# Kernel optimization log

Hardware: AMD Instinct MI355X
Metric: run time of the kernel (lower is better)

## Reference

```python
import jax, jax.numpy as jnp
import numpy as np

ROPE_THETA = 10000.0

def rope(x):
    # RoPE over the FULL model_dim (applied pre head-split, as in the source),
    # interleaved even/odd pairs. x: [B, S, D]
    B, S, D = x.shape
    half = D // 2
    inv_freq = 1.0 / (ROPE_THETA ** (jnp.arange(half, dtype=jnp.float32) * 2.0 / D))
    ang = jnp.arange(S, dtype=jnp.float32)[:, None] * inv_freq[None, :]  # [S, half]
    cos, sin = jnp.cos(ang), jnp.sin(ang)
    x1, x2 = x[..., 0::2], x[..., 1::2]
    r1 = x1 * cos - x2 * sin
    r2 = x1 * sin + x2 * cos
    return jnp.stack([r1, r2], axis=-1).reshape(B, S, D)


def setup_inputs() -> dict:
    key = jax.random.key(0)
    ks = jax.random.split(key, 9)
    B, S, D = 4, 2048, 768
    w = 0.02
    return {
        "X":  jax.random.normal(ks[0], (B, S, D), dtype=jnp.float32),
        "Wq": jax.random.normal(ks[1], (D, D), dtype=jnp.float32) * w,
        "bq": jnp.zeros((D,), dtype=jnp.float32),
        "Wk": jax.random.normal(ks[2], (D, D), dtype=jnp.float32) * w,
        "bk": jnp.zeros((D,), dtype=jnp.float32),
        "Wv": jax.random.normal(ks[3], (D, D), dtype=jnp.float32) * w,
        "bv": jnp.zeros((D,), dtype=jnp.float32),
        "Wo": jax.random.normal(ks[4], (D, D), dtype=jnp.float32) * w,
        "bo": jnp.zeros((D,), dtype=jnp.float32),
    }


def reference(X, Wq, bq, Wk, bk, Wv, bv, Wo, bo):
    NUM_HEADS = 12
    B, S, D = X.shape
    hd = D // NUM_HEADS

    q = rope(X @ Wq + bq)   # RoPE applied pre-split on full model_dim
    k = rope(X @ Wk + bk)
    v = X @ Wv + bv

    # Contiguous per-head slices == reshape to [B, S, H, hd]
    qh = q.reshape(B, S, NUM_HEADS, hd)
    kh = k.reshape(B, S, NUM_HEADS, hd)
    vh = v.reshape(B, S, NUM_HEADS, hd)

    scores = jnp.einsum('bqhd,bkhd->bhqk', qh, kh) / jnp.sqrt(jnp.float32(hd))
    causal = jnp.tril(jnp.ones((S, S), dtype=bool))
    scores = jnp.where(causal[None, None, :, :], scores, -jnp.inf)
    weights = jax.nn.softmax(scores, axis=-1)
    out = jnp.einsum('bhqk,bkhd->bqhd', weights, vh).reshape(B, S, D)
    return out @ Wo + bo
```

## Files before the change

kernel.cpp:

```cpp
#include <hip/hip_runtime.h>
#include <math.h>

#define D_MODEL 768
#define NUM_HEADS 12
#define HEAD_DIM 64
#define SEQ 2048
#define BATCH 4
#define MROWS (BATCH * SEQ)
#define HALF_D (D_MODEL / 2)

typedef __bf16 bf16x8 __attribute__((ext_vector_type(8)));
typedef __bf16 bf16x4 __attribute__((ext_vector_type(4)));
typedef float  f32x4  __attribute__((ext_vector_type(4)));

__device__ __forceinline__ void gload_lds16(const void* gp, void* lp) {
    __builtin_amdgcn_global_load_lds(
        (const __attribute__((address_space(1))) unsigned int*)gp,
        (__attribute__((address_space(3))) unsigned int*)lp, 16, 0, 0);
}

__global__ __launch_bounds__(256)
void prep(const float* __restrict__ X, __bf16* __restrict__ Xb,
          const float* __restrict__ W0, const float* __restrict__ W1,
          const float* __restrict__ W2, const float* __restrict__ W3,
          __bf16* __restrict__ T0, __bf16* __restrict__ T1,
          __bf16* __restrict__ T2, __bf16* __restrict__ T3)
{
    __shared__ float t[64][65];
    const int n   = blockIdx.x;
    const int tid = threadIdx.x;

    if (n < 3072) {
        size_t i = ((size_t)n * 256 + tid) * 8;
        float4 u = *(const float4*)(X + i);
        float4 v = *(const float4*)(X + i + 4);
        bf16x8 o;
        o[0]=(__bf16)u.x; o[1]=(__bf16)u.y; o[2]=(__bf16)u.z; o[3]=(__bf16)u.w;
        o[4]=(__bf16)v.x; o[5]=(__bf16)v.y; o[6]=(__bf16)v.z; o[7]=(__bf16)v.w;
        *(bf16x8*)(Xb + i) = o;
    } else {
        int m = n - 3072;
        int z = m / 144;
        int rem = m - z * 144;
        int by = rem / 12, bx = rem % 12;
        const float* W = z == 0 ? W0 : z == 1 ? W1 : z == 2 ? W2 : W3;
        __bf16*      T = z == 0 ? T0 : z == 1 ? T1 : z == 2 ? T2 : T3;

        const int r0 = by * 64, c0 = bx * 64;
        const int lx = tid & 63, g = tid >> 6;

        #pragma unroll
        for (int rr = 0; rr < 16; ++rr) {
            int r = g * 16 + rr;
            t[r][lx] = W[(size_t)(r0 + r) * D_MODEL + c0 + lx];
        }
        __syncthreads();

        const int nn = tid >> 2;
        const int kb = (tid & 3) * 16;
        bf16x8 o1, o2;
        #pragma unroll
        for (int mm = 0; mm < 8; ++mm) o1[mm] = (__bf16)t[kb + mm][nn];
        #pragma unroll
        for (int mm = 0; mm < 8; ++mm) o2[mm] = (__bf16)t[kb + 8 + mm][nn];
        __bf16* dst = T + (size_t)(c0 + nn) * D_MODEL + r0 + kb;
        *(bf16x8*)dst       = o1;
        *(bf16x8*)(dst + 8) = o2;
    }
}

__global__ __launch_bounds__(256)
void qkv_gemm(const __bf16* __restrict__ Xb,
              const __bf16* __restrict__ Wqt, const __bf16* __restrict__ Wkt,
              const __bf16* __restrict__ Wvt,
              const float* __restrict__ bq, const float* __restrict__ bk,
              const float* __restrict__ bv,
              __bf16* __restrict__ Qb, __bf16* __restrict__ Kb,
              __bf16* __restrict__ Vtb)
{
    __shared__ bf16x8 Asf[2][8][64];
    __shared__ bf16x8 Bsf[2][8][64];

    const int tid  = threadIdx.x;
    const int wv   = tid >> 6;
    const int ln   = tid & 63;
    const int t15  = ln & 15;
    const int quad = ln >> 4;
    const int wr = wv >> 1, wc = wv & 1;

    const int lin = blockIdx.x;
    const int c   = lin >> 6;
    const int r   = lin & 63;
    const int which = c / 6;
    const int col0  = (c % 6) * 128;
    const int row0  = r * 128;

    const __bf16* Wt  = which == 0 ? Wqt : which == 1 ? Wkt : Wvt;
    const float* bias = which == 0 ? bq  : which == 1 ? bk  : bv;

    f32x4 acc[4][4];
    #pragma unroll
    for (int i = 0; i < 4; ++i)
        #pragma unroll
        for (int j = 0; j < 4; ++j) acc[i][j] = (f32x4){0.f,0.f,0.f,0.f};

    const __bf16* a0 = Xb + (size_t)(row0 + 16 * wv       + t15) * D_MODEL + 8 * quad;
    const __bf16* a1 = Xb + (size_t)(row0 + 16 * (wv + 4) + t15) * D_MODEL + 8 * quad;
    const __bf16* b0 = Wt + (size_t)(col0 + 16 * wv       + t15) * D_MODEL + 8 * quad;
    const __bf16* b1 = Wt + (size_t)(col0 + 16 * (wv + 4) + t15) * D_MODEL + 8 * quad;

    for (int k0 = 0; k0 < D_MODEL; k0 += 64) {
        __syncthreads();
        #pragma unroll
        for (int ks = 0; ks < 2; ++ks) {
            const int kk = k0 + 32 * ks;
            gload_lds16(a0 + kk, &Asf[ks][wv][0]);
            gload_lds16(a1 + kk, &Asf[ks][wv + 4][0]);
            gload_lds16(b0 + kk, &Bsf[ks][wv][0]);
            gload_lds16(b1 + kk, &Bsf[ks][wv + 4][0]);
        }
        __syncthreads();

        #pragma unroll
        for (int ks = 0; ks < 2; ++ks) {
            bf16x8 af[4], bfr[4];
            #pragma unroll
            for (int i = 0; i < 4; ++i) af[i]  = Asf[ks][4 * wr + i][ln];
            #pragma unroll
            for (int j = 0; j < 4; ++j) bfr[j] = Bsf[ks][4 * wc + j][ln];
            #pragma unroll
            for (int i = 0; i < 4; ++i)
                #pragma unroll
                for (int j = 0; j < 4; ++j)
                    acc[i][j] = __builtin_amdgcn_mfma_f32_16x16x32_bf16(af[i], bfr[j], acc[i][j], 0, 0, 0);
        }
    }

    #pragma unroll
    for (int i = 0; i < 4; ++i) {
        const int rowb = row0 + 64 * wr + 16 * i + 4 * quad;
        #pragma unroll
        for (int j = 0; j < 4; ++j) {
            const int col = col0 + 64 * wc + 16 * j + t15;
            const float bval = bias[col];
            if (which < 2) {
                const int ne = col & ~1;
                const float fr = __expf((float)ne * (-9.210340371976184f / 768.0f));
                const float sgn = (col & 1) ? 1.0f : -1.0f;
                const float oscale = (which == 0) ? 0.125f : 1.0f;
                __bf16* dst = (which ? Kb : Qb);
                #pragma unroll
                for (int rr = 0; rr < 4; ++rr) {
                    const int rw = rowb + rr;
                    const int s  = rw & (SEQ - 1);
                    float val  = acc[i][j][rr] + bval;
                    float part = __shfl_xor(val, 1, 64);
                    float ang  = (float)s * fr;
                    float cs   = __cosf(ang);
                    float sn   = __sinf(ang);
                    dst[(size_t)rw * D_MODEL + col] = (__bf16)((val * cs + part * sgn * sn) * oscale);
                }
            } else {
                const int h = col >> 6, d = col & 63;
                const int bidx = rowb >> 11, s = rowb & (SEQ - 1);
                bf16x4 pk;
                #pragma unroll
                for (int rr = 0; rr < 4; ++rr) pk[rr] = (__bf16)(acc[i][j][rr] + bval);
                *(bf16x4*)(Vtb + ((size_t)(bidx * NUM_HEADS + h) * 64 + d) * SEQ + s) = pk;
            }
        }
    }
}

__global__ __launch_bounds__(256)
void out_gemm(const __bf16* __restrict__ Ab, const __bf16* __restrict__ Wt,
              const float* __restrict__ bias, float* __restrict__ Cout)
{
    __shared__ bf16x8 Asf[2][4][64];
    __shared__ bf16x8 Bsf[2][8][64];

    const int tid  = threadIdx.x;
    const int wv   = tid >> 6;
    const int ln   = tid & 63;
    const int t15  = ln & 15;
    const int quad = ln >> 4;
    const int wr = wv >> 1, wc = wv & 1;

    const int lin  = blockIdx.x;
    const int col0 = (lin >> 7) * 128;
    const int row0 = (lin & 127) * 64;

    f32x4 acc[2][4];
    #pragma unroll
    for (int i = 0; i < 2; ++i)
        #pragma unroll
        for (int j = 0; j < 4; ++j) acc[i][j] = (f32x4){0.f,0.f,0.f,0.f};

    for (int k0 = 0; k0 < D_MODEL; k0 += 64) {
        __syncthreads();
        #pragma unroll
        for (int u = 0; u < 6; ++u) {
            const int id = wv * 6 + u;
            const int ks = id / 12;
            const int w  = id % 12;
            if (w < 4) {
                const __bf16* src = Ab + (size_t)(row0 + 16 * w + t15) * D_MODEL
                                       + k0 + 32 * ks + 8 * quad;
                gload_lds16(src, &Asf[ks][w][0]);
            } else {
                const __bf16* src = Wt + (size_t)(col0 + 16 * (w - 4) + t15) * D_MODEL
                                       + k0 + 32 * ks + 8 * quad;
                gload_lds16(src, &Bsf[ks][w - 4][0]);
            }
        }
        __syncthreads();

        #pragma unroll
        for (int ks = 0; ks < 2; ++ks) {
            bf16x8 af[2], bfr[4];
            #pragma unroll
            for (int i = 0; i < 2; ++i) af[i]  = Asf[ks][2 * wr + i][ln];
            #pragma unroll
            for (int j = 0; j < 4; ++j) bfr[j] = Bsf[ks][4 * wc + j][ln];
            #pragma unroll
            for (int i = 0; i < 2; ++i)
                #pragma unroll
                for (int j = 0; j < 4; ++j)
                    acc[i][j] = __builtin_amdgcn_mfma_f32_16x16x32_bf16(af[i], bfr[j], acc[i][j], 0, 0, 0);
        }
    }

    #pragma unroll
    for (int i = 0; i < 2; ++i) {
        const int rowb = row0 + 32 * wr + 16 * i + 4 * quad;
        #pragma unroll
        for (int j = 0; j < 4; ++j) {
            const int col = col0 + 64 * wc + 16 * j + t15;
            const float bval = bias[col];
            #pragma unroll
            for (int rr = 0; rr < 4; ++rr)
                Cout[(size_t)(rowb + rr) * D_MODEL + col] = acc[i][j][rr] + bval;
        }
    }
}

__device__ __forceinline__ void attn_tile(
    const bf16x8 (*Kbuf)[64], const bf16x8 (*Vbuf)[64],
    __bf16 (*Psw)[72],
    bf16x8 aq0, bf16x8 aq1,
    f32x4* o, float* lacc,
    int ln, int t15, int quad, int j0, int qabs, bool domask)
{
    f32x4 s[4];
    #pragma unroll
    for (int c = 0; c < 4; ++c) {
        s[c] = (f32x4){0.f, 0.f, 0.f, 0.f};
        s[c] = __builtin_amdgcn_mfma_f32_16x16x32_bf16(aq0, Kbuf[c][ln],     s[c], 0, 0, 0);
        s[c] = __builtin_amdgcn_mfma_f32_16x16x32_bf16(aq1, Kbuf[4 + c][ln], s[c], 0, 0, 0);
    }

    float p[4][4];
    #pragma unroll
    for (int c = 0; c < 4; ++c)
        #pragma unroll
        for (int r = 0; r < 4; ++r) {
            float e = __expf(s[c][r]);
            if (domask && (j0 + 16 * c + t15 > qabs + r)) e = 0.f;
            p[c][r] = e;
            lacc[r] += e;
        }

    #pragma unroll
    for (int c = 0; c < 4; ++c)
        #pragma unroll
        for (int r = 0; r < 4; ++r)
            Psw[4 * quad + r][16 * c + t15] = (__bf16)p[c][r];
    __asm__ volatile("s_waitcnt lgkmcnt(0)" ::: "memory");

    bf16x8 ap0 = *(const bf16x8*)&Psw[t15][8 * quad];
    bf16x8 ap1 = *(const bf16x8*)&Psw[t15][32 + 8 * quad];

    #pragma unroll
    for (int c = 0; c < 4; ++c) {
        o[c] = __builtin_amdgcn_mfma_f32_16x16x32_bf16(ap0, Vbuf[c][ln],     o[c], 0, 0, 0);
        o[c] = __builtin_amdgcn_mfma_f32_16x16x32_bf16(ap1, Vbuf[4 + c][ln], o[c], 0, 0, 0);
    }
}

__global__ __launch_bounds__(512)
void attn_flash(const __bf16* __restrict__ Q, const __bf16* __restrict__ K,
                const __bf16* __restrict__ Vt, __bf16* __restrict__ O)
{
    __shared__ bf16x8 Kf[2][8][64];
    __shared__ bf16x8 Vf[2][8][64];
    __shared__ __bf16 Psb[8][16][72];

    const int tid  = threadIdx.x;
    const int wv   = tid >> 6;
    const int ln   = tid & 63;
    const int t15  = ln & 15;
    const int quad = ln >> 4;

    const int n  = blockIdx.x;
    const int qt = 15 - (n / 48);
    const int bh = n % 48;
    const int b  = bh / NUM_HEADS;
    const int h  = bh % NUM_HEADS;
    const int q0 = qt * 128;
    const int nt = (q0 >> 6) + 2;

    bf16x8 aq0, aq1;
    {
        const __bf16* qs = Q + (size_t)(b * SEQ + q0 + 16 * wv + t15) * D_MODEL + h * 64 + 8 * quad;
        aq0 = *(const bf16x8*)qs;
        aq1 = *(const bf16x8*)(qs + 32);
    }

    const __bf16* kp = K  + ((size_t)b * SEQ + 16 * (wv & 3) + t15) * D_MODEL
                          + h * 64 + 32 * (wv >> 2) + 8 * quad;
    const __bf16* vp = Vt + ((size_t)bh * 64 + 16 * (wv & 3) + t15) * SEQ
                          + 32 * (wv >> 2) + 8 * quad;

    f32x4 o[4];
    #pragma unroll
    for (int c = 0; c < 4; ++c) o[c] = (f32x4){0.f,0.f,0.f,0.f};
    float lacc[4] = {0.f, 0.f, 0.f, 0.f};
    const int qabs = q0 + 16 * wv + 4 * quad;
    const int wmax = q0 + 16 * wv + 15;

    gload_lds16(kp, &Kf[0][wv][0]);
    gload_lds16(vp, &Vf[0][wv][0]);

    int cur = 0;
    for (int it = 0; it < nt; ++it) {
        __syncthreads();
        if (it + 1 < nt) {
            const int jn = (it + 1) * 64;
            gload_lds16(kp + (size_t)jn * D_MODEL, &Kf[cur ^ 1][wv][0]);
            gload_lds16(vp + jn,                   &Vf[cur ^ 1][wv][0]);
        }
        const int j0 = it * 64;
        if (j0 <= wmax) {
            const bool domask = (j0 + 63) > (q0 + 16 * wv);
            attn_tile(Kf[cur], Vf[cur], Psb[wv], aq0, aq1, o, lacc,
                      ln, t15, quad, j0, qabs, domask);
        }
        cur ^= 1;
    }

    #pragma unroll
    for (int off = 1; off < 16; off <<= 1)
        #pragma unroll
        for (int r = 0; r < 4; ++r)
            lacc[r] += __shfl_xor(lacc[r], off, 64);

    float inv[4];
    #pragma unroll
    for (int r = 0; r < 4; ++r) inv[r] = 1.0f / lacc[r];
    #pragma unroll
    for (int c = 0; c < 4; ++c)
        #pragma unroll
        for (int r = 0; r < 4; ++r) {
            int row = qabs + r;
            O[(size_t)(b * SEQ + row) * D_MODEL + h * 64 + 16 * c + t15] = (__bf16)(o[c][r] * inv[r]);
        }
}

extern "C" void kernel_launch(void* const* d_in, const int* in_sizes, int n_in,
                              void* d_out, int out_size, void* d_ws, size_t ws_size,
                              hipStream_t stream) {
    const float* X  = (const float*)d_in[0];
    const float* Wq = (const float*)d_in[1];
    const float* bq = (const float*)d_in[2];
    const float* Wk = (const float*)d_in[3];
    const float* bk = (const float*)d_in[4];
    const float* Wv = (const float*)d_in[5];
    const float* bv = (const float*)d_in[6];
    const float* Wo = (const float*)d_in[7];
    const float* bo = (const float*)d_in[8];
    float* out = (float*)d_out;

    const size_t BSD = (size_t)MROWS * D_MODEL;
    const size_t WSZ = (size_t)D_MODEL * D_MODEL;

    __bf16* Xb  = (__bf16*)d_ws;
    __bf16* Qb  = Xb  + BSD;
    __bf16* Kb  = Qb  + BSD;
    __bf16* Vtb = Kb  + BSD;
    __bf16* Ob  = Vtb + BSD;
    __bf16* Wqt = Ob  + BSD;
    __bf16* Wkt = Wqt + WSZ;
    __bf16* Wvt = Wkt + WSZ;
    __bf16* Wot = Wvt + WSZ;

    prep<<<3648, 256, 0, stream>>>(X, Xb, Wq, Wk, Wv, Wo, Wqt, Wkt, Wvt, Wot);

    qkv_gemm<<<1152, 256, 0, stream>>>(Xb, Wqt, Wkt, Wvt, bq, bk, bv, Qb, Kb, Vtb);

    attn_flash<<<768, 512, 0, stream>>>(Qb, Kb, Vtb, Ob);

    out_gemm<<<768, 256, 0, stream>>>(Ob, Wot, bo, out);
}
```

Measured before the change: 250.7 us.

## Compute transposed scores so P feeds PV MFMA from registers, drop LDS round-trip

The attention tile now computes S^T (K as the A operand), so each lane's exp'd probabilities already form the A operand of a 16x16x16 f16 MFMA. The per-wave P shared-memory staging and its wait are removed, and V is stored and loaded in fp16 to match. The row-sum becomes a single scalar per lane, reduced across quads and redistributed at the end. The QKV epilogue also replaces per-element RoPE sin/cos with an angle-addition recurrence across four consecutive rows. Risks include fp16 precision for V and P, more small LDS reads of V, and accumulated error from the rotation recurrence.

```diff
diff --git a/kernel.cpp b/kernel.cpp
--- a/kernel.cpp
+++ b/kernel.cpp
@@ -9,9 +9,9 @@
 #define MROWS (BATCH * SEQ)
 #define HALF_D (D_MODEL / 2)
 
-typedef __bf16 bf16x8 __attribute__((ext_vector_type(8)));
-typedef __bf16 bf16x4 __attribute__((ext_vector_type(4)));
-typedef float  f32x4  __attribute__((ext_vector_type(4)));
+typedef __bf16    bf16x8 __attribute__((ext_vector_type(8)));
+typedef _Float16  f16x4  __attribute__((ext_vector_type(4)));
+typedef float     f32x4  __attribute__((ext_vector_type(4)));
 
 __device__ __forceinline__ void gload_lds16(const void* gp, void* lp) {
     __builtin_amdgcn_global_load_lds(
@@ -76,7 +76,7 @@
               const float* __restrict__ bq, const float* __restrict__ bk,
               const float* __restrict__ bv,
               __bf16* __restrict__ Qb, __bf16* __restrict__ Kb,
-              __bf16* __restrict__ Vtb)
+              _Float16* __restrict__ Vtb)
 {
     __shared__ bf16x8 Asf[2][8][64];
     __shared__ bf16x8 Bsf[2][8][64];
@@ -136,37 +136,49 @@
         }
     }
 
-    #pragma unroll
-    for (int i = 0; i < 4; ++i) {
-        const int rowb = row0 + 64 * wr + 16 * i + 4 * quad;
+    if (which < 2) {
+        __bf16* dst = (which ? Kb : Qb);
+        const float oscale = (which == 0) ? 0.125f : 1.0f;
         #pragma unroll
         for (int j = 0; j < 4; ++j) {
             const int col = col0 + 64 * wc + 16 * j + t15;
             const float bval = bias[col];
-            if (which < 2) {
-                const int ne = col & ~1;
-                const float fr = __expf((float)ne * (-9.210340371976184f / 768.0f));
-                const float sgn = (col & 1) ? 1.0f : -1.0f;
-                const float oscale = (which == 0) ? 0.125f : 1.0f;
-                __bf16* dst = (which ? Kb : Qb);
+            const int ne = col & ~1;
+            const float fr = __expf((float)ne * (-9.210340371976184f / 768.0f));
+            const float cf = __cosf(fr), sf = __sinf(fr);
+            const float sgn = (col & 1) ? 1.0f : -1.0f;
+            #pragma unroll
+            for (int i = 0; i < 4; ++i) {
+                const int rowb = row0 + 64 * wr + 16 * i + 4 * quad;
+                const int s0   = rowb & (SEQ - 1);
+                float ang = (float)s0 * fr;
+                float ca = __cosf(ang), sa = __sinf(ang);
                 #pragma unroll
                 for (int rr = 0; rr < 4; ++rr) {
                     const int rw = rowb + rr;
-                    const int s  = rw & (SEQ - 1);
                     float val  = acc[i][j][rr] + bval;
                     float part = __shfl_xor(val, 1, 64);
-                    float ang  = (float)s * fr;
-                    float cs   = __cosf(ang);
-                    float sn   = __sinf(ang);
-                    dst[(size_t)rw * D_MODEL + col] = (__bf16)((val * cs + part * sgn * sn) * oscale);
+                    dst[(size_t)rw * D_MODEL + col] = (__bf16)((val * ca + part * sgn * sa) * oscale);
+                    float cn = ca * cf - sa * sf;
+                    sa = sa * cf + ca * sf;
+                    ca = cn;
                 }
-            } else {
+            }
+        }
+    } else {
+        #pragma unroll
+        for (int i = 0; i < 4; ++i) {
+            const int rowb = row0 + 64 * wr + 16 * i + 4 * quad;
+            #pragma unroll
+            for (int j = 0; j < 4; ++j) {
+                const int col = col0 + 64 * wc + 16 * j + t15;
+                const float bval = bias[col];
                 const int h = col >> 6, d = col & 63;
                 const int bidx = rowb >> 11, s = rowb & (SEQ - 1);
-                bf16x4 pk;
+                f16x4 pk;
                 #pragma unroll
-                for (int rr = 0; rr < 4; ++rr) pk[rr] = (__bf16)(acc[i][j][rr] + bval);
-                *(bf16x4*)(Vtb + ((size_t)(bidx * NUM_HEADS + h) * 64 + d) * SEQ + s) = pk;
+                for (int rr = 0; rr < 4; ++rr) pk[rr] = (_Float16)(acc[i][j][rr] + bval);
+                *(f16x4*)(Vtb + ((size_t)(bidx * NUM_HEADS + h) * 64 + d) * SEQ + s) = pk;
             }
         }
     }
@@ -245,55 +257,48 @@
 }
 
 __device__ __forceinline__ void attn_tile(
-    const bf16x8 (*Kbuf)[64], const bf16x8 (*Vbuf)[64],
-    __bf16 (*Psw)[72],
+    const bf16x8 (*Kbuf)[64], const _Float16* Vbuf ,
     bf16x8 aq0, bf16x8 aq1,
-    f32x4* o, float* lacc,
-    int ln, int t15, int quad, int j0, int qabs, bool domask)
+    f32x4* o, float& lacc,
+    int ln, int t15, int quad, int j0, int qglob, bool domask)
 {
     f32x4 s[4];
     #pragma unroll
     for (int c = 0; c < 4; ++c) {
         s[c] = (f32x4){0.f, 0.f, 0.f, 0.f};
-        s[c] = __builtin_amdgcn_mfma_f32_16x16x32_bf16(aq0, Kbuf[c][ln],     s[c], 0, 0, 0);
-        s[c] = __builtin_amdgcn_mfma_f32_16x16x32_bf16(aq1, Kbuf[4 + c][ln], s[c], 0, 0, 0);
-    }
-
-    float p[4][4];
+        s[c] = __builtin_amdgcn_mfma_f32_16x16x32_bf16(Kbuf[c][ln],     aq0, s[c], 0, 0, 0);
+        s[c] = __builtin_amdgcn_mfma_f32_16x16x32_bf16(Kbuf[4 + c][ln], aq1, s[c], 0, 0, 0);
+    }
+
+    f16x4 pf[4];
     #pragma unroll
     for (int c = 0; c < 4; ++c)
         #pragma unroll
         for (int r = 0; r < 4; ++r) {
             float e = __expf(s[c][r]);
-            if (domask && (j0 + 16 * c + t15 > qabs + r)) e = 0.f;
-            p[c][r] = e;
-            lacc[r] += e;
-        }
-
-    #pragma unroll
-    for (int c = 0; c < 4; ++c)
-        #pragma unroll
-        for (int r = 0; r < 4; ++r)
-            Psw[4 * quad + r][16 * c + t15] = (__bf16)p[c][r];
-    __asm__ volatile("s_waitcnt lgkmcnt(0)" ::: "memory");
-
-    bf16x8 ap0 = *(const bf16x8*)&Psw[t15][8 * quad];
-    bf16x8 ap1 = *(const bf16x8*)&Psw[t15][32 + 8 * quad];
+            if (domask && (j0 + 16 * c + 4 * quad + r > qglob)) e = 0.f;
+            lacc += e;
+            pf[c][r] = (_Float16)e;
+        }
 
     #pragma unroll
     for (int c = 0; c < 4; ++c) {
-        o[c] = __builtin_amdgcn_mfma_f32_16x16x32_bf16(ap0, Vbuf[c][ln],     o[c], 0, 0, 0);
-        o[c] = __builtin_amdgcn_mfma_f32_16x16x32_bf16(ap1, Vbuf[4 + c][ln], o[c], 0, 0, 0);
+        const int lv = 16 * (2 * (c & 1) + (quad >> 1)) + t15;
+        const int jb = 4 * (quad & 1);
+        #pragma unroll
+        for (int cd = 0; cd < 4; ++cd) {
+            f16x4 vf = *(const f16x4*)&Vbuf[(size_t)(4 * (c >> 1) + cd) * 512 + lv * 8 + jb];
+            o[cd] = __builtin_amdgcn_mfma_f32_16x16x16f16(pf[c], vf, o[cd], 0, 0, 0);
+        }
     }
 }
 
 __global__ __launch_bounds__(512)
 void attn_flash(const __bf16* __restrict__ Q, const __bf16* __restrict__ K,
-                const __bf16* __restrict__ Vt, __bf16* __restrict__ O)
+                const _Float16* __restrict__ Vt, __bf16* __restrict__ O)
 {
-    __shared__ bf16x8 Kf[2][8][64];
-    __shared__ bf16x8 Vf[2][8][64];
-    __shared__ __bf16 Psb[8][16][72];
+    __shared__ bf16x8   Kf[2][8][64];
+    __shared__ _Float16 Vh[2][8][512];
 
     const int tid  = threadIdx.x;
     const int wv   = tid >> 6;
@@ -316,20 +321,20 @@
         aq1 = *(const bf16x8*)(qs + 32);
     }
 
-    const __bf16* kp = K  + ((size_t)b * SEQ + 16 * (wv & 3) + t15) * D_MODEL
-                          + h * 64 + 32 * (wv >> 2) + 8 * quad;
-    const __bf16* vp = Vt + ((size_t)bh * 64 + 16 * (wv & 3) + t15) * SEQ
-                          + 32 * (wv >> 2) + 8 * quad;
+    const __bf16*   kp = K  + ((size_t)b * SEQ + 16 * (wv & 3) + t15) * D_MODEL
+                            + h * 64 + 32 * (wv >> 2) + 8 * quad;
+    const _Float16* vp = Vt + ((size_t)bh * 64 + 16 * (wv & 3) + t15) * SEQ
+                            + 32 * (wv >> 2) + 8 * quad;
 
     f32x4 o[4];
     #pragma unroll
     for (int c = 0; c < 4; ++c) o[c] = (f32x4){0.f,0.f,0.f,0.f};
-    float lacc[4] = {0.f, 0.f, 0.f, 0.f};
-    const int qabs = q0 + 16 * wv + 4 * quad;
-    const int wmax = q0 + 16 * wv + 15;
+    float lacc = 0.f;
+    const int qglob = q0 + 16 * wv + t15;
+    const int wmax  = q0 + 16 * wv + 15;
 
     gload_lds16(kp, &Kf[0][wv][0]);
-    gload_lds16(vp, &Vf[0][wv][0]);
+    gload_lds16(vp, &Vh[0][wv][0]);
 
     int cur = 0;
     for (int it = 0; it < nt; ++it) {
@@ -337,31 +342,30 @@
         if (it + 1 < nt) {
             const int jn = (it + 1) * 64;
             gload_lds16(kp + (size_t)jn * D_MODEL, &Kf[cur ^ 1][wv][0]);
-            gload_lds16(vp + jn,                   &Vf[cur ^ 1][wv][0]);
+            gload_lds16(vp + jn,                   &Vh[cur ^ 1][wv][0]);
         }
         const int j0 = it * 64;
         if (j0 <= wmax) {
             const bool domask = (j0 + 63) > (q0 + 16 * wv);
-            attn_tile(Kf[cur], Vf[cur], Psb[wv], aq0, aq1, o, lacc,
-                      ln, t15, quad, j0, qabs, domask);
+            attn_tile(Kf[cur], &Vh[cur][0][0], aq0, aq1, o, lacc,
+                      ln, t15, quad, j0, qglob, domask);
         }
         cur ^= 1;
     }
 
-    #pragma unroll
-    for (int off = 1; off < 16; off <<= 1)
-        #pragma unroll
-        for (int r = 0; r < 4; ++r)
-            lacc[r] += __shfl_xor(lacc[r], off, 64);
+    lacc += __shfl_xor(lacc, 16, 64);
+    lacc += __shfl_xor(lacc, 32, 64);
 
     float inv[4];
     #pragma unroll
-    for (int r = 0; r < 4; ++r) inv[r] = 1.0f / lacc[r];
+    for (int r = 0; r < 4; ++r)
+        inv[r] = 1.0f / __shfl(lacc, 4 * quad + r, 64);
+
     #pragma unroll
     for (int c = 0; c < 4; ++c)
         #pragma unroll
         for (int r = 0; r < 4; ++r) {
-            int row = qabs + r;
+            int row = q0 + 16 * wv + 4 * quad + r;
             O[(size_t)(b * SEQ + row) * D_MODEL + h * 64 + 16 * c + t15] = (__bf16)(o[c][r] * inv[r]);
         }
 }
@@ -383,15 +387,15 @@
     const size_t BSD = (size_t)MROWS * D_MODEL;
     const size_t WSZ = (size_t)D_MODEL * D_MODEL;
 
-    __bf16* Xb  = (__bf16*)d_ws;
-    __bf16* Qb  = Xb  + BSD;
-    __bf16* Kb  = Qb  + BSD;
-    __bf16* Vtb = Kb  + BSD;
-    __bf16* Ob  = Vtb + BSD;
-    __bf16* Wqt = Ob  + BSD;
-    __bf16* Wkt = Wqt + WSZ;
-    __bf16* Wvt = Wkt + WSZ;
-    __bf16* Wot = Wvt + WSZ;
+    __bf16*   Xb  = (__bf16*)d_ws;
+    __bf16*   Qb  = Xb  + BSD;
+    __bf16*   Kb  = Qb  + BSD;
+    _Float16* Vtb = (_Float16*)(Kb + BSD);
+    __bf16*   Ob  = (__bf16*)(Vtb + BSD);
+    __bf16*   Wqt = Ob  + BSD;
+    __bf16*   Wkt = Wqt + WSZ;
+    __bf16*   Wvt = Wkt + WSZ;
+    __bf16*   Wot = Wvt + WSZ;
 
     prep<<<3648, 256, 0, stream>>>(X, Xb, Wq, Wk, Wv, Wo, Wqt, Wkt, Wvt, Wot);
 
```

Result: no change. 255.0 us (+1.7%).
